# Kernel optimization log

Hardware: AMD Instinct MI355X
Metric: run time of the kernel (lower is better)

The kernel has to match this reference:

```python
import jax, jax.numpy as jnp
import numpy as np

H = 256  # hidden_size
T = 4096  # sequence length
IN = 128  # input_size


def _lstm_dir(x_seq, Wih, Whh, b, reverse):
    # x_seq: [T, D_in]; Wih: [4H, D_in]; Whh: [4H, H]; b: [4H]
    xs = x_seq @ Wih.T + b  # precompute input projection [T, 4H]
    if reverse:
        xs = xs[::-1]

    def step(carry, xt):
        h, c = carry
        z = xt + h @ Whh.T
        i, f, g, o = jnp.split(z, 4, axis=-1)  # torch gate order i,f,g,o
        c = jax.nn.sigmoid(f) * c + jax.nn.sigmoid(i) * jnp.tanh(g)
        h = jax.nn.sigmoid(o) * jnp.tanh(c)
        return (h, c), h

    init = (jnp.zeros((H,), x_seq.dtype), jnp.zeros((H,), x_seq.dtype))
    _, hs = jax.lax.scan(step, init, xs)
    if reverse:
        hs = hs[::-1]
    return hs  # [T, H]


def _bilstm_layer(x_seq, Wih_f, Whh_f, b_f, Wih_b, Whh_b, b_b):
    hf = _lstm_dir(x_seq, Wih_f, Whh_f, b_f, False)
    hb = _lstm_dir(x_seq, Wih_b, Whh_b, b_b, True)
    return jnp.concatenate([hf, hb], axis=-1)  # [T, 2H]


def setup_inputs() -> dict:
    key = jax.random.key(0)
    ks = jax.random.split(key, 20)
    s = 1.0 / np.sqrt(H)

    def g(k, shape):
        return (jax.random.normal(k, shape, dtype=jnp.float32) * s)

    inp = {
        "x": jax.random.normal(ks[0], (1, T, IN), dtype=jnp.float32),
        # layer 0 (input dim IN), fwd / bwd directions; b = b_ih + b_hh folded
        "wih_l0f": g(ks[1], (4 * H, IN)), "whh_l0f": g(ks[2], (4 * H, H)), "b_l0f": g(ks[3], (4 * H,)),
        "wih_l0b": g(ks[4], (4 * H, IN)), "whh_l0b": g(ks[5], (4 * H, H)), "b_l0b": g(ks[6], (4 * H,)),
        # layer 1 (input dim 2H)
        "wih_l1f": g(ks[7], (4 * H, 2 * H)), "whh_l1f": g(ks[8], (4 * H, H)), "b_l1f": g(ks[9], (4 * H,)),
        "wih_l1b": g(ks[10], (4 * H, 2 * H)), "whh_l1b": g(ks[11], (4 * H, H)), "b_l1b": g(ks[12], (4 * H,)),
        # fc1: Linear(512, 256); fc2: Linear(256, 256)
        "fc1_w": g(ks[13], (256, 512)), "fc1_b": g(ks[14], (256,)),
        "fc2_w": g(ks[15], (256, 256)), "fc2_b": g(ks[16], (256,)),
    }
    return inp


def reference(x, wih_l0f, whh_l0f, b_l0f, wih_l0b, whh_l0b, b_l0b,
              wih_l1f, whh_l1f, b_l1f, wih_l1b, whh_l1b, b_l1b,
              fc1_w, fc1_b, fc2_w, fc2_b):
    xs = x[0]  # squeeze batch of 1 -> [T, IN]
    h1 = _bilstm_layer(xs, wih_l0f, whh_l0f, b_l0f, wih_l0b, whh_l0b, b_l0b)  # [T, 512]
    h2 = _bilstm_layer(h1, wih_l1f, whh_l1f, b_l1f, wih_l1b, whh_l1b, b_l1b)  # [T, 512]
    z = jnp.maximum(h2 @ fc1_w.T + fc1_b, 0.0)  # ReLU(fc1)
    e = z @ fc2_w.T + fc2_b  # [T, 256]
    # fused pairwise cosine similarity (replaces the per-row python loop)
    norms = jnp.linalg.norm(e, axis=1)  # [T]
    cs = (e @ e.T) / (norms[:, None] * norms[None, :])
    cs = jnp.maximum(cs, 1e-6)  # torch.clamp(min=1e-6)
    return 1.0 - cs  # [T, T]
```

## Files before the change

kernel.cpp:

```cpp
#include <hip/hip_runtime.h>
#include <hip/hip_fp16.h>

#define T_LEN 4096
#define HID   256
#define G4    1024
#define DIRSZ (1024 * 128)

typedef unsigned int u32;
typedef unsigned long long u64;
typedef _Float16 half2_t __attribute__((ext_vector_type(2)));

__device__ __forceinline__ float dot2f(u32 w, u32 h, float acc) {
#if __has_builtin(__builtin_amdgcn_fdot2)
    return __builtin_amdgcn_fdot2(__builtin_bit_cast(half2_t, w),
                                  __builtin_bit_cast(half2_t, h), acc, false);
#else
    __half2 wh = __builtin_bit_cast(__half2, w);
    __half2 hh = __builtin_bit_cast(__half2, h);
    float2 wf = __half22float2(wh), hf = __half22float2(hh);
    return acc + wf.x * hf.x + wf.y * hf.y;
#endif
}

__device__ __forceinline__ float qsum8(float v) {
    int i = __builtin_bit_cast(int, v);
    v += __builtin_bit_cast(float,
         __builtin_amdgcn_update_dpp(i, i, 0xB1, 0xF, 0xF, true));
    i = __builtin_bit_cast(int, v);
    v += __builtin_bit_cast(float,
         __builtin_amdgcn_update_dpp(i, i, 0x4E, 0xF, 0xF, true));
    i = __builtin_bit_cast(int, v);
    v += __builtin_bit_cast(float, __builtin_amdgcn_ds_swizzle(i, 0x101F));
    return v;
}

__device__ __forceinline__ u32 pack2(float a, float b) {
    unsigned short lo = __half_as_ushort(__float2half(a));
    unsigned short hi = __half_as_ushort(__float2half(b));
    return ((u32)hi << 16) | (u32)lo;
}

__device__ __forceinline__ void step_barrier() {
    asm volatile("s_waitcnt lgkmcnt(0)" ::: "memory");
    __builtin_amdgcn_s_barrier();
    __builtin_amdgcn_sched_barrier(0);
}

__global__ void k_zero(u32* __restrict__ p, int n) {
    int q = blockIdx.x * 256 + threadIdx.x;
    if (q < n) p[q] = 0u;
}

__global__ void k_transpose(const float* __restrict__ in, float* __restrict__ out,
                            int N, int K) {
    int q = blockIdx.x * 256 + threadIdx.x;
    if (q >= N * K) return;
    int n = q / K, k = q % K;
    out[(size_t)k * N + n] = in[q];
}

__global__ void k_pack_q8(const float* __restrict__ W, u32* __restrict__ out) {
    int idx = blockIdx.x * 256 + threadIdx.x;
    if (idx >= 1024 * 128) return;
    int widx = idx & 63;
    int tid  = (idx >> 6) & 511;
    int sl   = idx >> 15;
    int g = widx >> 4, rem = widx & 15;
    int bb = rem >> 2, i = rem & 3;
    int j = tid >> 3, q = tid & 7;
    int row = g * 256 + 64 * sl + j;
    int pair = 16 * q + 4 * ((bb + q) & 3) + i;
    out[idx] = pack2(W[row * 256 + 2 * pair], W[row * 256 + 2 * pair + 1]);
}

__global__ __launch_bounds__(256) void k_gemm(
    const float* __restrict__ A, const float* __restrict__ Wt,
    const float* __restrict__ bias, const float* __restrict__ norms,
    float* __restrict__ C, int M, int N, int K, int mode) {
    __shared__ float As[16 * 512];
    const int tid = threadIdx.x;
    const int m0 = blockIdx.x * 16;
    const int n  = blockIdx.y * 256 + tid;

    for (int i = tid; i < 16 * K; i += 256) As[i] = A[(size_t)m0 * K + i];
    __syncthreads();

    float acc[16];
#pragma unroll
    for (int m = 0; m < 16; ++m) acc[m] = 0.f;

#pragma unroll 4
    for (int k = 0; k < K; ++k) {
        float w = Wt[(size_t)k * N + n];
#pragma unroll
        for (int m = 0; m < 16; ++m) acc[m] += As[m * K + k] * w;
    }

    float bn = bias ? bias[n] : 0.f;
#pragma unroll
    for (int m = 0; m < 16; ++m) {
        float v = acc[m] + bn;
        if (mode == 1) v = fmaxf(v, 0.f);
        if (mode == 2) {
            float d = norms[m0 + m] * norms[n];
            v = 1.f - fmaxf(acc[m] / d, 1e-6f);
        }
        C[(size_t)(m0 + m) * N + n] = v;
    }
}

__global__ void k_norms(const float* __restrict__ e, float* __restrict__ norms) {
    int i = blockIdx.x, lane = threadIdx.x;
    float s = 0.f;
    for (int k = lane; k < 256; k += 64) { float v = e[i * 256 + k]; s += v * v; }
    for (int off = 32; off; off >>= 1) s += __shfl_down(s, off);
    if (lane == 0) norms[i] = sqrtf(s);
}

__global__ __launch_bounds__(512, 2) void k_scan_q8(
    const float* __restrict__ xs, const u32* __restrict__ rp,
    u64* __restrict__ ex, float* __restrict__ hout) {
    __shared__ alignas(16) u32 hb[2][128];

    const int bid = blockIdx.x;
    const int dir = bid & 1;
    const int s   = bid >> 1;
    const int tid = threadIdx.x;
    const int j   = tid >> 3;
    const int q   = tid & 7;
    const int gq  = q & 3;
    const int U   = 64 * s + j;

    xs += (size_t)dir * (T_LEN * G4);
    rp += (size_t)dir * DIRSZ;
    u64* exd = ex + dir * 256;

    u32 regw[64];
    {
        const uint4* rp4 = (const uint4*)(rp + (size_t)(s * 512 + tid) * 64);
#pragma unroll
        for (int p = 0; p < 16; ++p) {
            uint4 v = rp4[p];
            regw[4 * p + 0] = v.x; regw[4 * p + 1] = v.y;
            regw[4 * p + 2] = v.z; regw[4 * p + 3] = v.w;
        }
    }
    if (tid < 128) { hb[0][tid] = 0u; hb[1][tid] = 0u; }
    float cst = 0.f;
    __syncthreads();

    int tt = dir ? (T_LEN - 1) : 0;
    const int stp = dir ? -1 : 1;
    float xa = xs[(size_t)tt * G4 + (gq * 256 + U)];

    for (int t = 0; t < T_LEN; ++t) {
        const int cur = t & 1, nxt = cur ^ 1;
        int tn = (t + 1 < T_LEN) ? tt + stp : tt;
        float acc0 = (q == 0) ? xa : 0.f;
        float acc1 = (q == 1) ? xa : 0.f;
        float acc2 = (q == 2) ? xa : 0.f;
        float acc3 = (q == 3) ? xa : 0.f;
        xa = xs[(size_t)tn * G4 + (gq * 256 + U)];

        const u32* hq = &hb[cur][16 * q];
#pragma unroll
        for (int bb = 0; bb < 4; ++bb) {
            uint4 hv4 = *(const uint4*)&hq[4 * ((bb + q) & 3)];
            u32 hh[4] = { hv4.x, hv4.y, hv4.z, hv4.w };
#pragma unroll
            for (int i = 0; i < 4; ++i) {
                const int p = 4 * bb + i;
                acc0 = dot2f(regw[p],       hh[i], acc0);
                acc1 = dot2f(regw[16 + p],  hh[i], acc1);
                acc2 = dot2f(regw[32 + p],  hh[i], acc2);
                acc3 = dot2f(regw[48 + p],  hh[i], acc3);
            }
        }

        float zi = qsum8(acc0), zf = qsum8(acc1);
        float zg = qsum8(acc2), zo = qsum8(acc3);

        float si = 1.f / (1.f + __expf(-zi));
        float sf = 1.f / (1.f + __expf(-zf));
        float so = 1.f / (1.f + __expf(-zo));
        float tg = 1.f - 2.f / (__expf(2.f * zg) + 1.f);
        cst = sf * cst + si * tg;
        float th = 1.f - 2.f / (__expf(2.f * cst) + 1.f);
        float hv = so * th;

        float hn = __builtin_bit_cast(float,
            __builtin_amdgcn_ds_swizzle(__builtin_bit_cast(int, hv), 0x201F));

        if (q == 0)
            ((__half*)hb[nxt])[64 * s + j] = __float2half(hv);
        if (q == 0 && !(j & 1)) {
            u32 hp = pack2(hv, hn);
            u64 pay = ((u64)(u32)(t + 1) << 32) | (u64)hp;
            __hip_atomic_store(&exd[(cur * 4 + s) * 32 + (j >> 1)], pay,
                               __ATOMIC_RELAXED, __HIP_MEMORY_SCOPE_AGENT);
        }
        if (q == 1)
            hout[(size_t)tt * 512 + dir * 256 + U] = hv;
        if (tid < 96 && (t + 1 < T_LEN)) {
            int p_ = tid >> 5, w = tid & 31;
            int ps = (p_ < s) ? p_ : p_ + 1;
            u64 v;
            do {
                v = __hip_atomic_load(&exd[(cur * 4 + ps) * 32 + w],
                                      __ATOMIC_RELAXED, __HIP_MEMORY_SCOPE_AGENT);
            } while ((u32)(v >> 32) != (u32)(t + 1));
            hb[nxt][32 * ps + w] = (u32)v;
        }
        step_barrier();
        tt = tn;
    }
}

extern "C" void kernel_launch(void* const* d_in, const int* in_sizes, int n_in,
                              void* d_out, int out_size, void* d_ws, size_t ws_size,
                              hipStream_t stream) {
    const float* x       = (const float*)d_in[0];
    const float* wih_l0f = (const float*)d_in[1];
    const float* whh_l0f = (const float*)d_in[2];
    const float* b_l0f   = (const float*)d_in[3];
    const float* wih_l0b = (const float*)d_in[4];
    const float* whh_l0b = (const float*)d_in[5];
    const float* b_l0b   = (const float*)d_in[6];
    const float* wih_l1f = (const float*)d_in[7];
    const float* whh_l1f = (const float*)d_in[8];
    const float* b_l1f   = (const float*)d_in[9];
    const float* wih_l1b = (const float*)d_in[10];
    const float* whh_l1b = (const float*)d_in[11];
    const float* b_l1b   = (const float*)d_in[12];
    const float* fc1_w   = (const float*)d_in[13];
    const float* fc1_b   = (const float*)d_in[14];
    const float* fc2_w   = (const float*)d_in[15];
    const float* fc2_b   = (const float*)d_in[16];
    float* outp = (float*)d_out;

    char* ws = (char*)d_ws;
    size_t off = 0;
    auto alloc = [&](size_t nbytes) {
        char* p = ws + off;
        off += (nbytes + 255) & ~(size_t)255;
        return p;
    };
    float* xs0   = (float*)alloc((size_t)2 * T_LEN * G4 * 4);
    float* xs1   = (float*)alloc((size_t)2 * T_LEN * G4 * 4);
    float* h1    = (float*)alloc((size_t)T_LEN * 512 * 4);
    float* h2    = (float*)alloc((size_t)T_LEN * 512 * 4);
    float* zb    = (float*)alloc((size_t)T_LEN * 256 * 4);
    float* eb    = (float*)alloc((size_t)T_LEN * 256 * 4);
    float* etb   = (float*)alloc((size_t)T_LEN * 256 * 4);
    float* nrm   = (float*)alloc((size_t)T_LEN * 4);
    float* wt0f  = (float*)alloc((size_t)128 * 1024 * 4);
    float* wt0b  = (float*)alloc((size_t)128 * 1024 * 4);
    float* wt1f  = (float*)alloc((size_t)512 * 1024 * 4);
    float* wt1b  = (float*)alloc((size_t)512 * 1024 * 4);
    float* wtf1  = (float*)alloc((size_t)512 * 256 * 4);
    float* wtf2  = (float*)alloc((size_t)256 * 256 * 4);
    u32*   rpm0  = (u32*)alloc((size_t)2 * DIRSZ * 4);
    u32*   rpm1  = (u32*)alloc((size_t)2 * DIRSZ * 4);
    u64*   exA   = (u64*)alloc((size_t)512 * 8);
    u64*   exB   = (u64*)alloc((size_t)512 * 8);

    k_zero<<<8, 256, 0, stream>>>((u32*)exA, 2048);

    k_transpose<<<(1024 * 128 + 255) / 256, 256, 0, stream>>>(wih_l0f, wt0f, 1024, 128);
    k_transpose<<<(1024 * 128 + 255) / 256, 256, 0, stream>>>(wih_l0b, wt0b, 1024, 128);
    k_transpose<<<(1024 * 512 + 255) / 256, 256, 0, stream>>>(wih_l1f, wt1f, 1024, 512);
    k_transpose<<<(1024 * 512 + 255) / 256, 256, 0, stream>>>(wih_l1b, wt1b, 1024, 512);
    k_transpose<<<(256 * 512 + 255) / 256, 256, 0, stream>>>(fc1_w, wtf1, 256, 512);
    k_transpose<<<(256 * 256 + 255) / 256, 256, 0, stream>>>(fc2_w, wtf2, 256, 256);

    k_pack_q8<<<512, 256, 0, stream>>>(whh_l0f, rpm0);
    k_pack_q8<<<512, 256, 0, stream>>>(whh_l0b, rpm0 + DIRSZ);
    k_pack_q8<<<512, 256, 0, stream>>>(whh_l1f, rpm1);
    k_pack_q8<<<512, 256, 0, stream>>>(whh_l1b, rpm1 + DIRSZ);

    dim3 g1024(T_LEN / 16, 4);
    k_gemm<<<g1024, 256, 0, stream>>>(x, wt0f, b_l0f, nullptr, xs0, T_LEN, 1024, 128, 0);
    k_gemm<<<g1024, 256, 0, stream>>>(x, wt0b, b_l0b, nullptr, xs0 + (size_t)T_LEN * G4, T_LEN, 1024, 128, 0);
    k_scan_q8<<<8, 512, 0, stream>>>(xs0, rpm0, exA, h1);
    k_gemm<<<g1024, 256, 0, stream>>>(h1, wt1f, b_l1f, nullptr, xs1, T_LEN, 1024, 512, 0);
    k_gemm<<<g1024, 256, 0, stream>>>(h1, wt1b, b_l1b, nullptr, xs1 + (size_t)T_LEN * G4, T_LEN, 1024, 512, 0);
    k_scan_q8<<<8, 512, 0, stream>>>(xs1, rpm1, exB, h2);
    k_gemm<<<dim3(T_LEN / 16, 1), 256, 0, stream>>>(h2, wtf1, fc1_b, nullptr, zb, T_LEN, 256, 512, 1);
    k_gemm<<<dim3(T_LEN / 16, 1), 256, 0, stream>>>(zb, wtf2, fc2_b, nullptr, eb, T_LEN, 256, 256, 0);
    k_transpose<<<(T_LEN * 256 + 255) / 256, 256, 0, stream>>>(eb, etb, T_LEN, 256);
    k_norms<<<T_LEN, 64, 0, stream>>>(eb, nrm);
    k_gemm<<<dim3(T_LEN / 16, T_LEN / 256), 256, 0, stream>>>(eb, etb, nullptr, nrm, outp, T_LEN, T_LEN, 256, 2);
}
```

Before: 13.54 ms.

## Overlap local-slice recurrent dot product with remote hidden-state exchange in LSTM scan

The recurrent weights are repacked so each block first multiplies by its own slice of the hidden state, which is already in shared memory. That work runs before the block polls the other blocks' exchange slots. The exchange payload changes from packed half-pairs with a 32-bit step tag in a u64 to single halves with a 16-bit tag in a u32. The spin-wait now sits at the start of the next step rather than at the end of the current one. This is meant to hide inter-block synchronisation latency behind useful math, at the cost of a second block barrier per timestep and a narrower step tag.

```diff
diff --git a/kernel.cpp b/kernel.cpp
--- a/kernel.cpp
+++ b/kernel.cpp
@@ -59,18 +59,19 @@
     out[(size_t)k * N + n] = in[q];
 }
 
-__global__ void k_pack_q8(const float* __restrict__ W, u32* __restrict__ out) {
+__global__ void k_pack_s4(const float* __restrict__ W, u32* __restrict__ out) {
     int idx = blockIdx.x * 256 + threadIdx.x;
     if (idx >= 1024 * 128) return;
     int widx = idx & 63;
     int tid  = (idx >> 6) & 511;
     int sl   = idx >> 15;
-    int g = widx >> 4, rem = widx & 15;
-    int bb = rem >> 2, i = rem & 3;
-    int j = tid >> 3, q = tid & 7;
-    int row = g * 256 + 64 * sl + j;
-    int pair = 16 * q + 4 * ((bb + q) & 3) + i;
-    out[idx] = pack2(W[row * 256 + 2 * pair], W[row * 256 + 2 * pair + 1]);
+    int g = widx >> 4, tb = (widx >> 2) & 3, i = widx & 3;
+    int j = tid >> 3, q8 = tid & 7;
+    int U = 64 * sl + j;
+    int wsl = (tb == 0) ? sl : ((tb - 1 < sl) ? tb - 1 : tb);
+    int w = 32 * wsl + 4 * q8 + i;
+    int row = g * 256 + U;
+    out[idx] = pack2(W[row * 256 + 2 * w], W[row * 256 + 2 * w + 1]);
 }
 
 __global__ __launch_bounds__(256) void k_gemm(
@@ -117,9 +118,9 @@
     if (lane == 0) norms[i] = sqrtf(s);
 }
 
-__global__ __launch_bounds__(512, 2) void k_scan_q8(
+__global__ __launch_bounds__(512, 2) void k_scan_s4(
     const float* __restrict__ xs, const u32* __restrict__ rp,
-    u64* __restrict__ ex, float* __restrict__ hout) {
+    u32* __restrict__ ex, float* __restrict__ hout) {
     __shared__ alignas(16) u32 hb[2][128];
 
     const int bid = blockIdx.x;
@@ -127,13 +128,17 @@
     const int s   = bid >> 1;
     const int tid = threadIdx.x;
     const int j   = tid >> 3;
-    const int q   = tid & 7;
-    const int gq  = q & 3;
+    const int q8  = tid & 7;
+    const int gq  = q8 & 3;
     const int U   = 64 * s + j;
+
+    int ps0 = (0 < s) ? 0 : 1;
+    int ps1 = (1 < s) ? 1 : 2;
+    int ps2 = (2 < s) ? 2 : 3;
 
     xs += (size_t)dir * (T_LEN * G4);
     rp += (size_t)dir * DIRSZ;
-    u64* exd = ex + dir * 256;
+    u32* exd = ex + dir * 512;
 
     u32 regw[64];
     {
@@ -146,6 +151,7 @@
         }
     }
     if (tid < 128) { hb[0][tid] = 0u; hb[1][tid] = 0u; }
+    const int U2 = (tid < 64 * s) ? tid : tid + 64;
     float cst = 0.f;
     __syncthreads();
 
@@ -156,24 +162,70 @@
     for (int t = 0; t < T_LEN; ++t) {
         const int cur = t & 1, nxt = cur ^ 1;
         int tn = (t + 1 < T_LEN) ? tt + stp : tt;
-        float acc0 = (q == 0) ? xa : 0.f;
-        float acc1 = (q == 1) ? xa : 0.f;
-        float acc2 = (q == 2) ? xa : 0.f;
-        float acc3 = (q == 3) ? xa : 0.f;
+
+        u32 pv = 0;
+        if (t > 0 && tid < 192)
+            pv = __hip_atomic_load(&exd[cur * 256 + U2],
+                                   __ATOMIC_RELAXED, __HIP_MEMORY_SCOPE_AGENT);
+
+        float acc0 = (q8 == 0) ? xa : 0.f;
+        float acc1 = (q8 == 1) ? xa : 0.f;
+        float acc2 = (q8 == 2) ? xa : 0.f;
+        float acc3 = (q8 == 3) ? xa : 0.f;
         xa = xs[(size_t)tn * G4 + (gq * 256 + U)];
 
-        const u32* hq = &hb[cur][16 * q];
-#pragma unroll
-        for (int bb = 0; bb < 4; ++bb) {
-            uint4 hv4 = *(const uint4*)&hq[4 * ((bb + q) & 3)];
+        {
+            uint4 hv4 = *(const uint4*)&hb[cur][32 * s + 4 * q8];
             u32 hh[4] = { hv4.x, hv4.y, hv4.z, hv4.w };
 #pragma unroll
             for (int i = 0; i < 4; ++i) {
-                const int p = 4 * bb + i;
-                acc0 = dot2f(regw[p],       hh[i], acc0);
-                acc1 = dot2f(regw[16 + p],  hh[i], acc1);
-                acc2 = dot2f(regw[32 + p],  hh[i], acc2);
-                acc3 = dot2f(regw[48 + p],  hh[i], acc3);
+                acc0 = dot2f(regw[i],       hh[i], acc0);
+                acc1 = dot2f(regw[16 + i],  hh[i], acc1);
+                acc2 = dot2f(regw[32 + i],  hh[i], acc2);
+                acc3 = dot2f(regw[48 + i],  hh[i], acc3);
+            }
+        }
+
+        if (t > 0 && tid < 192) {
+            while ((pv >> 16) != (u32)t)
+                pv = __hip_atomic_load(&exd[cur * 256 + U2],
+                                       __ATOMIC_RELAXED, __HIP_MEMORY_SCOPE_AGENT);
+            ((__half*)hb[cur])[U2] =
+                __ushort_as_half((unsigned short)(pv & 0xffffu));
+        }
+        step_barrier();
+
+        {
+            uint4 hv4 = *(const uint4*)&hb[cur][32 * ps0 + 4 * q8];
+            u32 hh[4] = { hv4.x, hv4.y, hv4.z, hv4.w };
+#pragma unroll
+            for (int i = 0; i < 4; ++i) {
+                acc0 = dot2f(regw[4 + i],       hh[i], acc0);
+                acc1 = dot2f(regw[20 + i],  hh[i], acc1);
+                acc2 = dot2f(regw[36 + i],  hh[i], acc2);
+                acc3 = dot2f(regw[52 + i],  hh[i], acc3);
+            }
+        }
+        {
+            uint4 hv4 = *(const uint4*)&hb[cur][32 * ps1 + 4 * q8];
+            u32 hh[4] = { hv4.x, hv4.y, hv4.z, hv4.w };
+#pragma unroll
+            for (int i = 0; i < 4; ++i) {
+                acc0 = dot2f(regw[8 + i],       hh[i], acc0);
+                acc1 = dot2f(regw[24 + i],  hh[i], acc1);
+                acc2 = dot2f(regw[40 + i],  hh[i], acc2);
+                acc3 = dot2f(regw[56 + i],  hh[i], acc3);
+            }
+        }
+        {
+            uint4 hv4 = *(const uint4*)&hb[cur][32 * ps2 + 4 * q8];
+            u32 hh[4] = { hv4.x, hv4.y, hv4.z, hv4.w };
+#pragma unroll
+            for (int i = 0; i < 4; ++i) {
+                acc0 = dot2f(regw[12 + i],      hh[i], acc0);
+                acc1 = dot2f(regw[28 + i],  hh[i], acc1);
+                acc2 = dot2f(regw[44 + i],  hh[i], acc2);
+                acc3 = dot2f(regw[60 + i],  hh[i], acc3);
             }
         }
 
@@ -188,29 +240,16 @@
         float th = 1.f - 2.f / (__expf(2.f * cst) + 1.f);
         float hv = so * th;
 
-        float hn = __builtin_bit_cast(float,
-            __builtin_amdgcn_ds_swizzle(__builtin_bit_cast(int, hv), 0x201F));
-
-        if (q == 0)
-            ((__half*)hb[nxt])[64 * s + j] = __float2half(hv);
-        if (q == 0 && !(j & 1)) {
-            u32 hp = pack2(hv, hn);
-            u64 pay = ((u64)(u32)(t + 1) << 32) | (u64)hp;
-            __hip_atomic_store(&exd[(cur * 4 + s) * 32 + (j >> 1)], pay,
+        if (q8 == 0) {
+            unsigned short h16 = __half_as_ushort(__float2half(hv));
+            ((__half*)hb[nxt])[U] = __ushort_as_half(h16);
+            __hip_atomic_store(&exd[nxt * 256 + U],
+                               ((u32)(t + 1) << 16) | (u32)h16,
                                __ATOMIC_RELAXED, __HIP_MEMORY_SCOPE_AGENT);
         }
-        if (q == 1)
+        if (q8 == 1)
             hout[(size_t)tt * 512 + dir * 256 + U] = hv;
-        if (tid < 96 && (t + 1 < T_LEN)) {
-            int p_ = tid >> 5, w = tid & 31;
-            int ps = (p_ < s) ? p_ : p_ + 1;
-            u64 v;
-            do {
-                v = __hip_atomic_load(&exd[(cur * 4 + ps) * 32 + w],
-                                      __ATOMIC_RELAXED, __HIP_MEMORY_SCOPE_AGENT);
-            } while ((u32)(v >> 32) != (u32)(t + 1));
-            hb[nxt][32 * ps + w] = (u32)v;
-        }
+
         step_barrier();
         tt = tn;
     }
@@ -261,10 +300,10 @@
     float* wtf2  = (float*)alloc((size_t)256 * 256 * 4);
     u32*   rpm0  = (u32*)alloc((size_t)2 * DIRSZ * 4);
     u32*   rpm1  = (u32*)alloc((size_t)2 * DIRSZ * 4);
-    u64*   exA   = (u64*)alloc((size_t)512 * 8);
-    u64*   exB   = (u64*)alloc((size_t)512 * 8);
-
-    k_zero<<<8, 256, 0, stream>>>((u32*)exA, 2048);
+    u32*   exA   = (u32*)alloc((size_t)1024 * 4);
+    u32*   exB   = (u32*)alloc((size_t)1024 * 4);
+
+    k_zero<<<8, 256, 0, stream>>>(exA, 2048);
 
     k_transpose<<<(1024 * 128 + 255) / 256, 256, 0, stream>>>(wih_l0f, wt0f, 1024, 128);
     k_transpose<<<(1024 * 128 + 255) / 256, 256, 0, stream>>>(wih_l0b, wt0b, 1024, 128);
@@ -273,18 +312,18 @@
     k_transpose<<<(256 * 512 + 255) / 256, 256, 0, stream>>>(fc1_w, wtf1, 256, 512);
     k_transpose<<<(256 * 256 + 255) / 256, 256, 0, stream>>>(fc2_w, wtf2, 256, 256);
 
-    k_pack_q8<<<512, 256, 0, stream>>>(whh_l0f, rpm0);
-    k_pack_q8<<<512, 256, 0, stream>>>(whh_l0b, rpm0 + DIRSZ);
-    k_pack_q8<<<512, 256, 0, stream>>>(whh_l1f, rpm1);
-    k_pack_q8<<<512, 256, 0, stream>>>(whh_l1b, rpm1 + DIRSZ);
+    k_pack_s4<<<512, 256, 0, stream>>>(whh_l0f, rpm0);
+    k_pack_s4<<<512, 256, 0, stream>>>(whh_l0b, rpm0 + DIRSZ);
+    k_pack_s4<<<512, 256, 0, stream>>>(whh_l1f, rpm1);
+    k_pack_s4<<<512, 256, 0, stream>>>(whh_l1b, rpm1 + DIRSZ);
 
     dim3 g1024(T_LEN / 16, 4);
     k_gemm<<<g1024, 256, 0, stream>>>(x, wt0f, b_l0f, nullptr, xs0, T_LEN, 1024, 128, 0);
     k_gemm<<<g1024, 256, 0, stream>>>(x, wt0b, b_l0b, nullptr, xs0 + (size_t)T_LEN * G4, T_LEN, 1024, 128, 0);
-    k_scan_q8<<<8, 512, 0, stream>>>(xs0, rpm0, exA, h1);
+    k_scan_s4<<<8, 512, 0, stream>>>(xs0, rpm0, exA, h1);
     k_gemm<<<g1024, 256, 0, stream>>>(h1, wt1f, b_l1f, nullptr, xs1, T_LEN, 1024, 512, 0);
     k_gemm<<<g1024, 256, 0, stream>>>(h1, wt1b, b_l1b, nullptr, xs1 + (size_t)T_LEN * G4, T_LEN, 1024, 512, 0);
-    k_scan_q8<<<8, 512, 0, stream>>>(xs1, rpm1, exB, h2);
+    k_scan_s4<<<8, 512, 0, stream>>>(xs1, rpm1, exB, h2);
     k_gemm<<<dim3(T_LEN / 16, 1), 256, 0, stream>>>(h2, wtf1, fc1_b, nullptr, zb, T_LEN, 256, 512, 1);
     k_gemm<<<dim3(T_LEN / 16, 1), 256, 0, stream>>>(zb, wtf2, fc2_b, nullptr, eb, T_LEN, 256, 256, 0);
     k_transpose<<<(T_LEN * 256 + 255) / 256, 256, 0, stream>>>(eb, etb, T_LEN, 256);
```

Result: faster. 12.65 ms (-6.6%).
